# Kernel optimization log

Hardware: AMD Instinct MI355X
Metric: run time of the kernel (lower is better)

Reference implementation:

```python
import jax, jax.numpy as jnp
import numpy as np
import math

H = 32      # num attention heads
KV = 8      # num key/value heads
D = 64      # head dim
ROPE_BASE = 10000.0


def _rope_cos_sin(seq_len, dtype):
    inv_freq = 1.0 / (ROPE_BASE ** (jnp.arange(0, D, 2, dtype=jnp.float32) / D))
    t = jnp.arange(seq_len, dtype=jnp.float32)
    freqs = jnp.einsum('i,j->ij', t, inv_freq)          # [S, D/2]
    emb = jnp.concatenate([freqs, freqs], axis=-1)       # [S, D]
    return jnp.cos(emb).astype(dtype)[None, None], jnp.sin(emb).astype(dtype)[None, None]


def _rotate_half(x):
    x1, x2 = x[..., : D // 2], x[..., D // 2:]
    return jnp.concatenate([-x2, x1], axis=-1)


def setup_inputs() -> dict:
    key = jax.random.key(0)
    ks = jax.random.split(key, 5)
    B, S, Hid = 1, 2048, 2048
    hidden_states = jax.random.normal(ks[0], (B, S, Hid), dtype=jnp.float32)
    Wq = jax.random.normal(ks[1], (Hid, H * D), dtype=jnp.float32) * (1.0 / math.sqrt(Hid))
    Wk = jax.random.normal(ks[2], (Hid, KV * D), dtype=jnp.float32) * (1.0 / math.sqrt(Hid))
    Wv = jax.random.normal(ks[3], (Hid, KV * D), dtype=jnp.float32) * (1.0 / math.sqrt(Hid))
    Wo = jax.random.normal(ks[4], (H * D, Hid), dtype=jnp.float32) * (1.0 / math.sqrt(H * D))
    # additive causal mask
    causal = jnp.tril(jnp.ones((S, S), dtype=bool))
    attention_mask = jnp.where(causal, 0.0, -1e9).astype(jnp.float32)[None, None]
    return {"hidden_states": hidden_states, "Wq": Wq, "Wk": Wk, "Wv": Wv,
            "Wo": Wo, "attention_mask": attention_mask}


def reference(hidden_states, Wq, Wk, Wv, Wo, attention_mask):
    B, S, _ = hidden_states.shape
    groups = H // KV
    # projections -> [B, heads, S, D]
    q = (hidden_states @ Wq).reshape(B, S, H, D).transpose(0, 2, 1, 3)
    k = (hidden_states @ Wk).reshape(B, S, KV, D).transpose(0, 2, 1, 3)
    v = (hidden_states @ Wv).reshape(B, S, KV, D).transpose(0, 2, 1, 3)
    # RoPE
    cos, sin = _rope_cos_sin(S, q.dtype)
    q = q * cos + _rotate_half(q) * sin
    k = k * cos + _rotate_half(k) * sin
    # GQA head expansion (repeat_interleave along head axis)
    k = jnp.repeat(k, groups, axis=1)
    v = jnp.repeat(v, groups, axis=1)
    # scaled dot-product attention (eager)
    scores = jnp.einsum('bhqd,bhkd->bhqk', q, k) / math.sqrt(D)
    scores = scores + attention_mask
    probs = jax.nn.softmax(scores.astype(jnp.float32), axis=-1).astype(q.dtype)
    attn = jnp.einsum('bhqk,bhkd->bhqd', probs, v)
    attn = attn.transpose(0, 2, 1, 3).reshape(B, S, H * D)
    return attn @ Wo
```

## Files before the change

### kernel.cpp

```cpp
#include <hip/hip_runtime.h>
#include <hip/hip_bf16.h>
#include <math.h>

#define S_LEN 2048
#define HID   2048
#define NH    32
#define NKV   8
#define HD    64
#define KVW   (NKV * HD)

typedef __attribute__((ext_vector_type(8))) short bf16x8;
typedef __attribute__((ext_vector_type(4))) float f32x4;
typedef unsigned short u16;

__device__ __forceinline__ u16 f2bf(float f) {
    return (u16)((__builtin_bit_cast(unsigned, f) + 0x8000u) >> 16);
}
__device__ __forceinline__ float bf2f(u16 v) {
    unsigned u = ((unsigned)v) << 16;
    return __builtin_bit_cast(float, u);
}
__device__ __forceinline__ unsigned pack2bf(float a, float b) {
    unsigned ua = __builtin_bit_cast(unsigned, a) + 0x8000u;
    unsigned ub = __builtin_bit_cast(unsigned, b) + 0x8000u;
    return (ua >> 16) | (ub & 0xFFFF0000u);
}
__device__ __forceinline__ void stage16(const u16* g, u16* lds_base) {
    __builtin_amdgcn_global_load_lds((const __attribute__((address_space(1))) void*)g,
                                     (__attribute__((address_space(3))) void*)lds_base, 16, 0, 0);
}

__global__ __launch_bounds__(256) void cvt_bf16x8_kernel(const float* __restrict__ X,
                                                         u16* __restrict__ Y, int n8) {
    int i = blockIdx.x * 256 + threadIdx.x;
    if (i >= n8) return;
    const float4* p = (const float4*)(X + (size_t)i * 8);
    float4 a = p[0], b = p[1];
    uint4 o;
    o.x = pack2bf(a.x, a.y);
    o.y = pack2bf(a.z, a.w);
    o.z = pack2bf(b.x, b.y);
    o.w = pack2bf(b.z, b.w);
    *(uint4*)(Y + (size_t)i * 8) = o;
}

__global__ __launch_bounds__(256) void transpose_cvt4(const float* __restrict__ Wq,
                                                      const float* __restrict__ Wk,
                                                      const float* __restrict__ Wv,
                                                      const float* __restrict__ Wo,
                                                      u16* __restrict__ WqkvT,
                                                      u16* __restrict__ WoT) {
    const float* X; u16* Y; int C;
    const int z = blockIdx.z;
    if (z == 0)      { X = Wq; Y = WqkvT;                        C = HID; }
    else if (z == 1) { X = Wo; Y = WoT;                          C = HID; }
    else if (z == 2) { X = Wk; Y = WqkvT + (size_t)2048 * HID;   C = KVW; }
    else             { X = Wv; Y = WqkvT + (size_t)2560 * HID;   C = KVW; }
    const int c0 = blockIdx.x * 32, r0 = blockIdx.y * 32;
    if (c0 >= C) return;
    __shared__ float T[32][33];
    const int tx = threadIdx.x & 31, ty = threadIdx.x >> 5;
#pragma unroll
    for (int i = 0; i < 4; i++)
        T[ty + 8 * i][tx] = X[(size_t)(r0 + ty + 8 * i) * C + c0 + tx];
    __syncthreads();
#pragma unroll
    for (int i = 0; i < 4; i++)
        Y[(size_t)(c0 + ty + 8 * i) * HID + r0 + tx] = f2bf(T[tx][ty + 8 * i]);
}

template <int EPI>
__global__ __launch_bounds__(512, 4) void gemm_bf16(const u16* __restrict__ A,
                                                    const u16* __restrict__ Bt,
                                                    float* __restrict__ C,
                                                    u16* __restrict__ Qh,
                                                    u16* __restrict__ Kh,
                                                    u16* __restrict__ Vt,
                                                    int K) {
    __shared__ u16 As[2][128 * 64];
    __shared__ u16 Bs[2][128 * 64];

    const int t = threadIdx.x;
    const int w = t >> 6, lane = t & 63;
    const int qd = lane >> 4, r = lane & 15;
    const int wm = w >> 2, wn = w & 3;
    const int bm = blockIdx.y * 128, bn = blockIdx.x * 128;
    const bool kblk = (EPI == 1) && (bn >= 2048) && (bn < 2560);

    f32x4 acc[4][2];
#pragma unroll
    for (int i = 0; i < 4; i++)
#pragma unroll
        for (int j = 0; j < 2; j++) {
            acc[i][j][0] = 0.f; acc[i][j][1] = 0.f; acc[i][j][2] = 0.f; acc[i][j][3] = 0.f;
        }

    auto stageAB = [&](int k0, u16* dstA, u16* dstB) {
#pragma unroll
        for (int rd = 0; rd < 2; rd++) {
            const u16* ga = A + (size_t)(bm + w * 16 + r) * K + k0 + rd * 32 + qd * 8;
            stage16(ga, dstA + (w * 2 + rd) * 512);
            const u16* gb = Bt + (size_t)(bn + w * 16 + r) * K + k0 + rd * 32 + qd * 8;
            stage16(gb, dstB + (w * 2 + rd) * 512);
        }
    };

    stageAB(0, As[0], Bs[0]);
    __syncthreads();
    int cur = 0;

    for (int k0 = 0; k0 < K; k0 += 64) {
        if (k0 + 64 < K)
            stageAB(k0 + 64, As[cur ^ 1], Bs[cur ^ 1]);

#pragma unroll
        for (int ss = 0; ss < 2; ss++) {
            bf16x8 af[4], bfr[2];
#pragma unroll
            for (int i = 0; i < 4; i++)
                af[i] = *(const bf16x8*)&As[cur][((wm * 4 + i) * 2 + ss) * 512 + lane * 8];
#pragma unroll
            for (int j = 0; j < 2; j++) {
                int tile = kblk ? ((wn >> 1) * 4 + (wn & 1) + 2 * j) : (wn * 2 + j);
                bfr[j] = *(const bf16x8*)&Bs[cur][(tile * 2 + ss) * 512 + lane * 8];
            }
#pragma unroll
            for (int i = 0; i < 4; i++)
#pragma unroll
                for (int j = 0; j < 2; j++)
                    acc[i][j] = __builtin_amdgcn_mfma_f32_16x16x32_bf16(af[i], bfr[j], acc[i][j], 0, 0, 0);
        }

        __syncthreads();
        cur ^= 1;
    }

    const int row0 = bm + wm * 64;
    if (EPI == 0) {
#pragma unroll
        for (int i = 0; i < 4; i++)
#pragma unroll
            for (int j = 0; j < 2; j++)
#pragma unroll
                for (int reg = 0; reg < 4; reg++)
                    C[(size_t)(row0 + i * 16 + qd * 4 + reg) * HID + bn + wn * 32 + j * 16 + r] =
                        acc[i][j][reg];
    } else if (bn < 2048) {
#pragma unroll
        for (int i = 0; i < 4; i++)
#pragma unroll
            for (int j = 0; j < 2; j++)
#pragma unroll
                for (int reg = 0; reg < 4; reg++)
                    Qh[(size_t)(row0 + i * 16 + qd * 4 + reg) * HID + bn + wn * 32 + j * 16 + r] =
                        f2bf(acc[i][j][reg]);
    } else if (kblk) {
        const int c0 = (wn & 1) * 16 + r;
        const int hb = (bn - 2048) + (wn >> 1) * 64;
        const float inv = __expf(-(float)c0 * 0.2878231366242596f);
#pragma unroll
        for (int i = 0; i < 4; i++)
#pragma unroll
            for (int reg = 0; reg < 4; reg++) {
                int srow = row0 + i * 16 + qd * 4 + reg;
                float ang = (float)srow * inv;
                float cs = cosf(ang), sn = sinf(ang);
                float k1 = acc[i][0][reg], k2 = acc[i][1][reg];
                size_t o = (size_t)srow * KVW + hb + c0;
                Kh[o]      = f2bf(k1 * cs - k2 * sn);
                Kh[o + 32] = f2bf(k2 * cs + k1 * sn);
            }
    } else {
#pragma unroll
        for (int i = 0; i < 4; i++)
#pragma unroll
            for (int j = 0; j < 2; j++) {
                int nrel = (bn - 2560) + wn * 32 + j * 16 + r;
                int m0 = row0 + i * 16 + qd * 4;
                ushort4 v;
                v.x = f2bf(acc[i][j][0]); v.y = f2bf(acc[i][j][1]);
                v.z = f2bf(acc[i][j][2]); v.w = f2bf(acc[i][j][3]);
                *(ushort4*)(Vt + (size_t)nrel * S_LEN + m0) = v;
            }
    }
}

__global__ __launch_bounds__(512, 6) void attn_mfma(const u16* __restrict__ Qh,
                                                    const u16* __restrict__ K,
                                                    const u16* __restrict__ Vt,
                                                    u16* __restrict__ O) {
    __shared__ u16 Kbuf[2][4096];
    __shared__ u16 Vbuf[2][4096];
    __shared__ u16 P_lds[8][16][72];

    const int w    = threadIdx.x >> 6;
    const int lane = threadIdx.x & 63;
    const int qd   = lane >> 4;
    const int r    = lane & 15;
    const int qb   = 15 - (int)blockIdx.x;
    const int h    = blockIdx.y;
    const int kvh  = h >> 2;
    const int q0w  = qb * 128 + w * 16;

    const u16* qrow = Qh + (size_t)(q0w + r) * (NH * HD) + h * HD;
    bf16x8 qlo = *(const bf16x8*)(qrow + qd * 8);
    bf16x8 qhi = *(const bf16x8*)(qrow + 32 + qd * 8);
    float y1[8], y2[8];
    const float spos = (float)(q0w + r);
    const float LN1E4_OVER_32 = 0.2878231366242596f;
#pragma unroll
    for (int i = 0; i < 8; i++) {
        int jj = qd * 8 + i;
        float x1 = bf2f((u16)qlo[i]);
        float x2 = bf2f((u16)qhi[i]);
        float inv = __expf(-(float)jj * LN1E4_OVER_32);
        float ang = spos * inv;
        float c = cosf(ang), sn = sinf(ang);
        y1[i] = (x1 * c - x2 * sn) * 0.125f;
        y2[i] = (x2 * c + x1 * sn) * 0.125f;
    }
    bf16x8 qfrag[2];
    {
        union { unsigned u[4]; bf16x8 v; } a, b;
#pragma unroll
        for (int i = 0; i < 4; i++) {
            a.u[i] = pack2bf(y1[2 * i], y1[2 * i + 1]);
            b.u[i] = pack2bf(y2[2 * i], y2[2 * i + 1]);
        }
        qfrag[0] = a.v; qfrag[1] = b.v;
    }

    bf16x8 ones;
    {
        union { u16 s[8]; bf16x8 v; } u;
#pragma unroll
        for (int i = 0; i < 8; i++) u.s[i] = 0x3F80;
        ones = u.v;
    }

    f32x4 oacc[4];
    f32x4 lacc;
#pragma unroll
    for (int i = 0; i < 4; i++) { oacc[i][0]=0.f; oacc[i][1]=0.f; oacc[i][2]=0.f; oacc[i][3]=0.f; }
    lacc[0]=0.f; lacc[1]=0.f; lacc[2]=0.f; lacc[3]=0.f;

    const int ktmax = 2 * qb + 1;

#define STAGE_K(kt_, buf_)                                                        \
    {                                                                             \
        const u16* g = K + (size_t)((kt_) * 64 + (w >> 1) * 16 + r) * KVW         \
                         + kvh * HD + (w & 1) * 32 + qd * 8;                      \
        stage16(g, &Kbuf[buf_][w * 512]);                                         \
    }
#define STAGE_V(kt_, buf_)                                                        \
    {                                                                             \
        const u16* g = Vt + (size_t)(kvh * HD + (w >> 1) * 16 + r) * S_LEN        \
                          + (kt_) * 64 + (w & 1) * 32 + qd * 8;                   \
        stage16(g, &Vbuf[buf_][w * 512]);                                         \
    }

    STAGE_K(0, 0);
    STAGE_V(0, 0);
    __syncthreads();
    int cur = 0;

    for (int kt = 0; kt <= ktmax; kt++) {
        if (kt < ktmax) {
            STAGE_K(kt + 1, cur ^ 1);
            STAGE_V(kt + 1, cur ^ 1);
        }

        f32x4 s[4];
#pragma unroll
        for (int nt = 0; nt < 4; nt++) {
            bf16x8 kf0 = *(const bf16x8*)&Kbuf[cur][(nt * 2 + 0) * 512 + lane * 8];
            bf16x8 kf1 = *(const bf16x8*)&Kbuf[cur][(nt * 2 + 1) * 512 + lane * 8];
            f32x4 z; z[0]=0.f; z[1]=0.f; z[2]=0.f; z[3]=0.f;
            z = __builtin_amdgcn_mfma_f32_16x16x32_bf16(qfrag[0], kf0, z, 0, 0, 0);
            s[nt] = __builtin_amdgcn_mfma_f32_16x16x32_bf16(qfrag[1], kf1, z, 0, 0, 0);
        }

        if (kt * 64 + 63 > q0w) {
#pragma unroll
            for (int nt = 0; nt < 4; nt++) {
                int key = kt * 64 + nt * 16 + r;
#pragma unroll
                for (int reg = 0; reg < 4; reg++) {
                    int qg = q0w + qd * 4 + reg;
                    if (key > qg) s[nt][reg] = -1e30f;
                }
            }
        }

#pragma unroll
        for (int nt = 0; nt < 4; nt++)
#pragma unroll
            for (int reg = 0; reg < 4; reg++)
                P_lds[w][qd * 4 + reg][nt * 16 + r] = f2bf(__expf(s[nt][reg]));


#pragma unroll
        for (int c = 0; c < 2; c++) {
            bf16x8 pf = *(const bf16x8*)&P_lds[w][r][c * 32 + qd * 8];
            lacc = __builtin_amdgcn_mfma_f32_16x16x32_bf16(pf, ones, lacc, 0, 0, 0);
#pragma unroll
            for (int ntd = 0; ntd < 4; ntd++) {
                bf16x8 vf = *(const bf16x8*)&Vbuf[cur][(ntd * 2 + c) * 512 + lane * 8];
                oacc[ntd] = __builtin_amdgcn_mfma_f32_16x16x32_bf16(pf, vf, oacc[ntd], 0, 0, 0);
            }
        }

        __syncthreads();
        cur ^= 1;
    }
#undef STAGE_K
#undef STAGE_V

    float rl[4];
#pragma unroll
    for (int reg = 0; reg < 4; reg++) rl[reg] = 1.f / lacc[reg];
#pragma unroll
    for (int ntd = 0; ntd < 4; ntd++)
#pragma unroll
        for (int reg = 0; reg < 4; reg++)
            O[(size_t)(q0w + qd * 4 + reg) * (NH * HD) + h * HD + ntd * 16 + r] =
                f2bf(oacc[ntd][reg] * rl[reg]);
}

extern "C" void kernel_launch(void* const* d_in, const int* in_sizes, int n_in,
                              void* d_out, int out_size, void* d_ws, size_t ws_size,
                              hipStream_t stream) {
    const float* hidden = (const float*)d_in[0];
    const float* Wq = (const float*)d_in[1];
    const float* Wk = (const float*)d_in[2];
    const float* Wv = (const float*)d_in[3];
    const float* Wo = (const float*)d_in[4];
    float* out = (float*)d_out;

    char* ws = (char*)d_ws;
    const size_t MB = 1024 * 1024;
    u16* Hh     = (u16*)(ws + 0 * MB);
    u16* WqkvT  = (u16*)(ws + 8 * MB);
    u16* WoT    = (u16*)(ws + 20 * MB);
    u16* Qh     = (u16*)(ws + 28 * MB);
    u16* Kh     = (u16*)(ws + 36 * MB);
    u16* Vt     = (u16*)(ws + 38 * MB);
    u16* Ob     = WqkvT;

    cvt_bf16x8_kernel<<<(S_LEN * HID / 8 + 255) / 256, 256, 0, stream>>>(hidden, Hh, S_LEN * HID / 8);
    transpose_cvt4<<<dim3(HID / 32, HID / 32, 4), 256, 0, stream>>>(Wq, Wk, Wv, Wo, WqkvT, WoT);

    gemm_bf16<1><<<dim3(3072 / 128, S_LEN / 128), 512, 0, stream>>>(Hh, WqkvT, nullptr, Qh, Kh, Vt, HID);

    attn_mfma<<<dim3(S_LEN / 128, NH), 512, 0, stream>>>(Qh, Kh, Vt, Ob);

    gemm_bf16<0><<<dim3(HID / 128, S_LEN / 128), 512, 0, stream>>>(Ob, WoT, out, nullptr, nullptr, nullptr, HID);
}
```

Measured before the change: 285.0 us.

## Triple-buffer GEMM with 32-wide K slabs and single-buffer V in attention

```diff
diff --git a/kernel.cpp b/kernel.cpp
--- a/kernel.cpp
+++ b/kernel.cpp
@@ -70,15 +70,15 @@
 }
 
 template <int EPI>
-__global__ __launch_bounds__(512, 4) void gemm_bf16(const u16* __restrict__ A,
+__global__ __launch_bounds__(512, 6) void gemm_bf16(const u16* __restrict__ A,
                                                     const u16* __restrict__ Bt,
                                                     float* __restrict__ C,
                                                     u16* __restrict__ Qh,
                                                     u16* __restrict__ Kh,
                                                     u16* __restrict__ Vt,
                                                     int K) {
-    __shared__ u16 As[2][128 * 64];
-    __shared__ u16 Bs[2][128 * 64];
+    __shared__ u16 As[3][128 * 32];
+    __shared__ u16 Bs[3][128 * 32];
 
     const int t = threadIdx.x;
     const int w = t >> 6, lane = t & 63;
@@ -86,6 +86,7 @@
     const int wm = w >> 2, wn = w & 3;
     const int bm = blockIdx.y * 128, bn = blockIdx.x * 128;
     const bool kblk = (EPI == 1) && (bn >= 2048) && (bn < 2560);
+    const int NT = K >> 5;
 
     f32x4 acc[4][2];
 #pragma unroll
@@ -95,44 +96,46 @@
             acc[i][j][0] = 0.f; acc[i][j][1] = 0.f; acc[i][j][2] = 0.f; acc[i][j][3] = 0.f;
         }
 
-    auto stageAB = [&](int k0, u16* dstA, u16* dstB) {
-#pragma unroll
-        for (int rd = 0; rd < 2; rd++) {
-            const u16* ga = A + (size_t)(bm + w * 16 + r) * K + k0 + rd * 32 + qd * 8;
-            stage16(ga, dstA + (w * 2 + rd) * 512);
-            const u16* gb = Bt + (size_t)(bn + w * 16 + r) * K + k0 + rd * 32 + qd * 8;
-            stage16(gb, dstB + (w * 2 + rd) * 512);
-        }
+    auto stage_slab = [&](int kt) {
+        const int k0 = kt * 32;
+        const int s = kt % 3;
+        const u16* ga = A + (size_t)(bm + w * 16 + r) * K + k0 + qd * 8;
+        stage16(ga, &As[s][w * 512]);
+        const u16* gb = Bt + (size_t)(bn + w * 16 + r) * K + k0 + qd * 8;
+        stage16(gb, &Bs[s][w * 512]);
     };
 
-    stageAB(0, As[0], Bs[0]);
-    __syncthreads();
-    int cur = 0;
-
-    for (int k0 = 0; k0 < K; k0 += 64) {
-        if (k0 + 64 < K)
-            stageAB(k0 + 64, As[cur ^ 1], Bs[cur ^ 1]);
-
-#pragma unroll
-        for (int ss = 0; ss < 2; ss++) {
-            bf16x8 af[4], bfr[2];
-#pragma unroll
-            for (int i = 0; i < 4; i++)
-                af[i] = *(const bf16x8*)&As[cur][((wm * 4 + i) * 2 + ss) * 512 + lane * 8];
-#pragma unroll
-            for (int j = 0; j < 2; j++) {
-                int tile = kblk ? ((wn >> 1) * 4 + (wn & 1) + 2 * j) : (wn * 2 + j);
-                bfr[j] = *(const bf16x8*)&Bs[cur][(tile * 2 + ss) * 512 + lane * 8];
-            }
-#pragma unroll
-            for (int i = 0; i < 4; i++)
-#pragma unroll
-                for (int j = 0; j < 2; j++)
-                    acc[i][j] = __builtin_amdgcn_mfma_f32_16x16x32_bf16(af[i], bfr[j], acc[i][j], 0, 0, 0);
-        }
-
-        __syncthreads();
-        cur ^= 1;
+    auto compute_slab = [&](int kt) {
+        const int s = kt % 3;
+        bf16x8 af[4], bfr[2];
+#pragma unroll
+        for (int i = 0; i < 4; i++)
+            af[i] = *(const bf16x8*)&As[s][(wm * 4 + i) * 512 + lane * 8];
+#pragma unroll
+        for (int j = 0; j < 2; j++) {
+            int tile = kblk ? ((wn >> 1) * 4 + (wn & 1) + 2 * j) : (wn * 2 + j);
+            bfr[j] = *(const bf16x8*)&Bs[s][tile * 512 + lane * 8];
+        }
+#pragma unroll
+        for (int i = 0; i < 4; i++)
+#pragma unroll
+            for (int j = 0; j < 2; j++)
+                acc[i][j] = __builtin_amdgcn_mfma_f32_16x16x32_bf16(af[i], bfr[j], acc[i][j], 0, 0, 0);
+    };
+
+    stage_slab(0);
+    stage_slab(1);
+    asm volatile("s_waitcnt vmcnt(2)" ::: "memory");
+    __builtin_amdgcn_s_barrier();
+
+    for (int kt = 0; kt < NT; ++kt) {
+        if (kt + 2 < NT) stage_slab(kt + 2);
+        compute_slab(kt);
+        if (kt + 2 < NT)
+            asm volatile("s_waitcnt vmcnt(2) lgkmcnt(0)" ::: "memory");
+        else
+            asm volatile("s_waitcnt vmcnt(0) lgkmcnt(0)" ::: "memory");
+        __builtin_amdgcn_s_barrier();
     }
 
     const int row0 = bm + wm * 64;
@@ -190,7 +193,7 @@
                                                     const u16* __restrict__ Vt,
                                                     u16* __restrict__ O) {
     __shared__ u16 Kbuf[2][4096];
-    __shared__ u16 Vbuf[2][4096];
+    __shared__ u16 Vbuf[4096];
     __shared__ u16 P_lds[8][16][72];
 
     const int w    = threadIdx.x >> 6;
@@ -252,23 +255,20 @@
                          + kvh * HD + (w & 1) * 32 + qd * 8;                      \
         stage16(g, &Kbuf[buf_][w * 512]);                                         \
     }
-#define STAGE_V(kt_, buf_)                                                        \
+#define STAGE_V(kt_)                                                              \
     {                                                                             \
         const u16* g = Vt + (size_t)(kvh * HD + (w >> 1) * 16 + r) * S_LEN        \
                           + (kt_) * 64 + (w & 1) * 32 + qd * 8;                   \
-        stage16(g, &Vbuf[buf_][w * 512]);                                         \
+        stage16(g, &Vbuf[w * 512]);                                               \
     }
 
     STAGE_K(0, 0);
-    STAGE_V(0, 0);
     __syncthreads();
     int cur = 0;
 
     for (int kt = 0; kt <= ktmax; kt++) {
-        if (kt < ktmax) {
-            STAGE_K(kt + 1, cur ^ 1);
-            STAGE_V(kt + 1, cur ^ 1);
-        }
+        STAGE_V(kt);
+        if (kt < ktmax) STAGE_K(kt + 1, cur ^ 1);
 
         f32x4 s[4];
 #pragma unroll
@@ -298,6 +298,7 @@
             for (int reg = 0; reg < 4; reg++)
                 P_lds[w][qd * 4 + reg][nt * 16 + r] = f2bf(__expf(s[nt][reg]));
 
+        __syncthreads();
 
 #pragma unroll
         for (int c = 0; c < 2; c++) {
@@ -305,7 +306,7 @@
             lacc = __builtin_amdgcn_mfma_f32_16x16x32_bf16(pf, ones, lacc, 0, 0, 0);
 #pragma unroll
             for (int ntd = 0; ntd < 4; ntd++) {
-                bf16x8 vf = *(const bf16x8*)&Vbuf[cur][(ntd * 2 + c) * 512 + lane * 8];
+                bf16x8 vf = *(const bf16x8*)&Vbuf[(ntd * 2 + c) * 512 + lane * 8];
                 oacc[ntd] = __builtin_amdgcn_mfma_f32_16x16x32_bf16(pf, vf, oacc[ntd], 0, 0, 0);
             }
         }
```

After: 289.7 us. About the same (+1.7%).
